# Performance work log

Hardware: AMD Instinct MI355X
Metric: run time of the kernel (lower is better)

Reference implementation:

```python
import jax, jax.numpy as jnp
import numpy as np
from jax import lax

B, S, I = 128, 256, 128          # batch, seq_len, input_size
CTX, OUT = 256, 128              # context_input_size, output_size
CPM, NM = 1024, 4                # center_size_per_module, num_modules
CENTER = NM * CPM
IN_SIZES = [I + CTX, CTX, CTX, CTX]          # only module 0 sees the input
HID = [CPM, CPM, CPM, CPM + OUT]             # last module also emits output


def setup_inputs() -> dict:
    key = jax.random.key(0)
    ks = jax.random.split(key, 4 + 5 * NM)
    d = {
        "inputs": jax.random.normal(ks[0], (B, 1, S, I), jnp.float32),
        "center_init": jax.random.normal(ks[1], (NM, B, CPM), jnp.float32),
        "mod_init": jax.random.normal(ks[2], (NM - 1, B, CPM), jnp.float32),
        "mod_init_last": jax.random.normal(ks[3], (B, CPM + OUT), jnp.float32),
    }
    for i in range(NM):
        k = ks[4 + 5 * i: 4 + 5 * (i + 1)]
        d[f"pm{i}"] = jax.random.normal(k[0], (CENTER, CTX), jnp.float32) * 0.02
        d[f"wih{i}"] = jax.random.normal(k[1], (3 * HID[i], IN_SIZES[i]), jnp.float32) * 0.05
        d[f"whh{i}"] = jax.random.normal(k[2], (3 * HID[i], HID[i]), jnp.float32) * 0.05
        d[f"bih{i}"] = jnp.zeros((3 * HID[i],), jnp.float32)
        d[f"bhh{i}"] = jnp.zeros((3 * HID[i],), jnp.float32)
    return d


def _gru(x, h, wih, whh, bih, bhh):
    # PyTorch GRUCell semantics
    gi = x @ wih.T + bih
    gh = h @ whh.T + bhh
    ir, iz, inn = jnp.split(gi, 3, axis=1)
    hr, hz, hn = jnp.split(gh, 3, axis=1)
    r = jax.nn.sigmoid(ir + hr)
    z = jax.nn.sigmoid(iz + hz)
    n = jnp.tanh(inn + r * hn)
    return (1.0 - z) * n + z * h


def _forward(inputs, center_init, mod_init, mod_init_last, pms, wihs, whhs, bihs, bhhs):
    xs = jnp.swapaxes(inputs[:, 0], 0, 1)  # [S, B, I]

    def step(carry, x_t):
        centers, mods, mod_last = carry  # [NM,B,CPM], [NM-1,B,CPM], [B,CPM+OUT]
        # torch.cat(prev_center_states, dim=1): module-major concat -> [B, NM*CPM]
        center_state = jnp.reshape(jnp.swapaxes(centers, 0, 1), (centers.shape[1], -1))
        new_centers, new_mods = [], []
        out = new_mod_last = None
        for i in range(NM):
            ctx = center_state @ pms[i]                       # [B, CTX]
            xin = jnp.concatenate([x_t, ctx], axis=1) if i == 0 else ctx
            h_prev = mod_last if i == NM - 1 else mods[i]
            h = _gru(xin, h_prev, wihs[i], whhs[i], bihs[i], bhhs[i])
            if i == NM - 1:
                out = h[:, :OUT]                              # split([output, center_feat])
                new_centers.append(h[:, OUT:])
                new_mod_last = h
            else:
                new_centers.append(h)
                new_mods.append(h)
        return (jnp.stack(new_centers), jnp.stack(new_mods), new_mod_last), out

    _, ys = lax.scan(step, (center_init, mod_init, mod_init_last), xs)
    return jnp.swapaxes(ys, 0, 1)  # [B, S, OUT]


def reference(inputs, center_init, mod_init, mod_init_last,
              pm0, pm1, pm2, pm3,
              wih0, wih1, wih2, wih3,
              whh0, whh1, whh2, whh3,
              bih0, bih1, bih2, bih3,
              bhh0, bhh1, bhh2, bhh3):
    return _forward(inputs, center_init, mod_init, mod_init_last,
                    (pm0, pm1, pm2, pm3),
                    (wih0, wih1, wih2, wih3),
                    (whh0, whh1, whh2, whh3),
                    (bih0, bih1, bih2, bih3),
                    (bhh0, bhh1, bhh2, bhh3))
```

## Files before the change

### kernel.cpp

```cpp
#include <hip/hip_runtime.h>
#include <hip/hip_bf16.h>

typedef _Float16 f16;
typedef f16  f16x8 __attribute__((ext_vector_type(8)));
typedef float f32x4 __attribute__((ext_vector_type(4)));

__device__ __forceinline__ f16x8 ld8h(const f16* p){ return *reinterpret_cast<const f16x8*>(p); }
__device__ __forceinline__ void fsplit(float x, f16* hi, f16* lo){
    f16 h=(f16)x; *hi=h; *lo=(f16)((x-(float)h)*4096.0f);
}
__device__ __forceinline__ size_t fragoff(int n, int k, int Kc){
    return ((size_t)(n>>4)*Kc + (k>>5))*512 + (size_t)((((k&31)>>3)*16 + (n&15))*8 + (k&7));
}

constexpr size_t NXE   = 128ull*256*128;
constexpr size_t NPM   = 1024ull*4096;
constexpr size_t NWIH0 = 3072ull*384;
constexpr size_t NWIH12= 3072ull*256;
constexpr size_t NWIH3 = 3456ull*256;
constexpr size_t NWHH  = 3072ull*1024;
constexpr size_t NWHH3 = 3456ull*1152;
constexpr size_t NCEN  = 128ull*4096;
constexpr size_t NCTX  = 128ull*1024;
constexpr size_t NHMX  = 128ull*1152;

constexpr size_t OFF_XH    = 0;
constexpr size_t OFF_XL    = OFF_XH + NXE*2;
constexpr size_t OFF_PMH   = OFF_XL + NXE*2;
constexpr size_t OFF_PML   = OFF_PMH + NPM*2;
constexpr size_t OFF_WIHH0 = OFF_PML + NPM*2;
constexpr size_t OFF_WIHH1 = OFF_WIHH0 + NWIH0*2;
constexpr size_t OFF_WIHH2 = OFF_WIHH1 + NWIH12*2;
constexpr size_t OFF_WIHH3 = OFF_WIHH2 + NWIH12*2;
constexpr size_t OFF_WIHL0 = OFF_WIHH3 + NWIH3*2;
constexpr size_t OFF_WIHL1 = OFF_WIHL0 + NWIH0*2;
constexpr size_t OFF_WIHL2 = OFF_WIHL1 + NWIH12*2;
constexpr size_t OFF_WIHL3 = OFF_WIHL2 + NWIH12*2;
constexpr size_t OFF_WHHH0 = OFF_WIHL3 + NWIH3*2;
constexpr size_t OFF_WHHH1 = OFF_WHHH0 + NWHH*2;
constexpr size_t OFF_WHHH2 = OFF_WHHH1 + NWHH*2;
constexpr size_t OFF_WHHH3 = OFF_WHHH2 + NWHH*2;
constexpr size_t OFF_WHHL0 = OFF_WHHH3 + NWHH3*2;
constexpr size_t OFF_WHHL1 = OFF_WHHL0 + NWHH*2;
constexpr size_t OFF_WHHL2 = OFF_WHHL1 + NWHH*2;
constexpr size_t OFF_WHHL3 = OFF_WHHL2 + NWHH*2;
constexpr size_t OFF_CENH  = OFF_WHHL3 + NWHH3*2;
constexpr size_t OFF_CENL  = OFF_CENH + 2*NCEN*2;
constexpr size_t OFF_CTXH  = OFF_CENL + 2*NCEN*2;
constexpr size_t OFF_CTXL  = OFF_CTXH + NCTX*2;
constexpr size_t OFF_HH    = OFF_CTXL + NCTX*2;
constexpr size_t OFF_HL    = OFF_HH + 8*NHMX*2;
constexpr size_t OFF_HF    = OFF_HL + 8*NHMX*2;
constexpr size_t WS_NEED   = OFF_HF + 8*NHMX*4;

__device__ __forceinline__ f16* hh_ptr(char* ws,int p,int i){ return (f16*)(ws+OFF_HH+((size_t)(p*4+i))*NHMX*2); }
__device__ __forceinline__ f16* hl_ptr(char* ws,int p,int i){ return (f16*)(ws+OFF_HL+((size_t)(p*4+i))*NHMX*2); }
__device__ __forceinline__ float* hf_ptr(char* ws,int p,int i){ return (float*)(ws+OFF_HF+((size_t)(p*4+i))*NHMX*4); }

__global__ void k_repack_w(const float* __restrict__ src, f16* __restrict__ hi,
                           f16* __restrict__ lo, int K){
    int n = blockIdx.x;
    const float* row = src + (size_t)n*K;
    int Kc = K >> 5;
    for (int k8 = threadIdx.x*8; k8 < K; k8 += 2048) {
        f16x8 hv, lv;
        #pragma unroll
        for (int e = 0; e < 8; ++e) { f16 a,b; fsplit(row[k8+e], &a, &b); hv[e]=a; lv[e]=b; }
        size_t d = fragoff(n, k8, Kc);
        *reinterpret_cast<f16x8*>(hi + d) = hv;
        *reinterpret_cast<f16x8*>(lo + d) = lv;
    }
}

__global__ void k_repack_pm(const float* __restrict__ p0, const float* __restrict__ p1,
                            const float* __restrict__ p2, const float* __restrict__ p3,
                            f16* __restrict__ hi, f16* __restrict__ lo){
    int k0 = blockIdx.x * 8;
    for (int c = threadIdx.x; c < 1024; c += 256) {
        int i = c >> 8, nl = c & 255;
        const float* p = (i==0?p0 : i==1?p1 : i==2?p2 : p3);
        f16x8 hv, lv;
        #pragma unroll
        for (int e = 0; e < 8; ++e) { f16 a,b; fsplit(p[(size_t)(k0+e)*256 + nl], &a, &b); hv[e]=a; lv[e]=b; }
        #pragma unroll
        for (int e = 0; e < 8; ++e) { size_t d = fragoff(c, k0+e, 128); hi[d]=hv[e]; lo[d]=lv[e]; }
    }
}

__global__ void k_repack_x(const float* __restrict__ src, f16* __restrict__ hi, f16* __restrict__ lo){
    size_t g = ((size_t)blockIdx.x*256 + threadIdx.x) * 8;
    if (g >= NXE) return;
    int m = (int)(g >> 15), t = (int)((g >> 7) & 255), d0 = (int)(g & 127);
    f16x8 hv, lv;
    #pragma unroll
    for (int e = 0; e < 8; ++e) { f16 a,b; fsplit(src[g+e], &a, &b); hv[e]=a; lv[e]=b; }
    size_t d = (size_t)t*16384 + fragoff(m, d0, 4);
    *reinterpret_cast<f16x8*>(hi + d) = hv;
    *reinterpret_cast<f16x8*>(lo + d) = lv;
}

__global__ void k_init_cen(const float* __restrict__ ci, char* ws){
    size_t g = ((size_t)blockIdx.x*256 + threadIdx.x) * 8;
    if (g >= 4ull*128*1024) return;
    int i = (int)(g >> 17), b = (int)((g >> 10) & 127), c = (int)(g & 1023);
    f16* hi = (f16*)(ws + OFF_CENH);
    f16* lo = (f16*)(ws + OFF_CENL);
    f16x8 hv, lv;
    #pragma unroll
    for (int e = 0; e < 8; ++e) { f16 a,bb; fsplit(ci[g+e], &a, &bb); hv[e]=a; lv[e]=bb; }
    size_t d = fragoff(b, i*1024 + c, 128);
    *reinterpret_cast<f16x8*>(hi + d) = hv;
    *reinterpret_cast<f16x8*>(lo + d) = lv;
}

__global__ void k_init_mod(const float* __restrict__ mi, char* ws){
    size_t g = ((size_t)blockIdx.x*256 + threadIdx.x) * 8;
    if (g >= 3ull*128*1024) return;
    int i = (int)(g >> 17), b = (int)((g >> 10) & 127), j = (int)(g & 1023);
    float* hf = hf_ptr(ws, 0, i);
    f16 *hh = hh_ptr(ws, 0, i), *hl = hl_ptr(ws, 0, i);
    f16x8 hv, lv;
    #pragma unroll
    for (int e = 0; e < 8; ++e) {
        float v = mi[g+e]; hf[(size_t)b*1024 + j + e] = v;
        f16 a,bb; fsplit(v, &a, &bb); hv[e]=a; lv[e]=bb;
    }
    size_t d = fragoff(b, j, 32);
    *reinterpret_cast<f16x8*>(hh + d) = hv;
    *reinterpret_cast<f16x8*>(hl + d) = lv;
}

__global__ void k_init_last(const float* __restrict__ ml, char* ws){
    int b = blockIdx.x;
    float* hf = hf_ptr(ws, 0, 3);
    f16 *hh = hh_ptr(ws, 0, 3), *hl = hl_ptr(ws, 0, 3);
    for (int j = threadIdx.x*8; j < 1152; j += 2048) {
        f16x8 hv, lv;
        #pragma unroll
        for (int e = 0; e < 8; ++e) {
            float v = ml[(size_t)b*1152 + j + e]; hf[(size_t)b*1152 + j + e] = v;
            f16 a,bb; fsplit(v, &a, &bb); hv[e]=a; lv[e]=bb;
        }
        size_t d = fragoff(b, j, 36);
        *reinterpret_cast<f16x8*>(hh + d) = hv;
        *reinterpret_cast<f16x8*>(hl + d) = lv;
    }
}

__global__ __launch_bounds__(512) void k_ctx(char* ws, int par){
    __shared__ float red[8][32][17];
    const f16* cenh = (const f16*)(ws + OFF_CENH) + (size_t)par*NCEN;
    const f16* cenl = (const f16*)(ws + OFF_CENL) + (size_t)par*NCEN;
    const f16* pmh  = (const f16*)(ws + OFF_PMH);
    const f16* pml  = (const f16*)(ws + OFF_PML);
    int tid = threadIdx.x, lane = tid & 63, wv = tid >> 6;
    int bm = blockIdx.x >> 6, bn = blockIdx.x & 63;
    size_t lb = (size_t)lane*8;
    size_t a0 = ((size_t)(bm*2)*128 + wv*16)*512 + lb;
    size_t a1 = a0 + 128*512;
    size_t bb = ((size_t)bn*128 + wv*16)*512 + lb;
    f32x4 h0={},h1={},c0={},c1={};
    #pragma unroll 4
    for (int kc = 0; kc < 16; ++kc) {
        f16x8 bh = ld8h(pmh + bb + kc*512), bl = ld8h(pml + bb + kc*512);
        f16x8 ah0 = ld8h(cenh + a0 + kc*512), al0 = ld8h(cenl + a0 + kc*512);
        f16x8 ah1 = ld8h(cenh + a1 + kc*512), al1 = ld8h(cenl + a1 + kc*512);
        h0 = __builtin_amdgcn_mfma_f32_16x16x32_f16(ah0, bh, h0, 0,0,0);
        c0 = __builtin_amdgcn_mfma_f32_16x16x32_f16(al0, bh, c0, 0,0,0);
        c0 = __builtin_amdgcn_mfma_f32_16x16x32_f16(ah0, bl, c0, 0,0,0);
        h1 = __builtin_amdgcn_mfma_f32_16x16x32_f16(ah1, bh, h1, 0,0,0);
        c1 = __builtin_amdgcn_mfma_f32_16x16x32_f16(al1, bh, c1, 0,0,0);
        c1 = __builtin_amdgcn_mfma_f32_16x16x32_f16(ah1, bl, c1, 0,0,0);
    }
    int rg = lane >> 4, fr = lane & 15;
    const float inv = 1.0f/4096.0f;
    #pragma unroll
    for (int rr = 0; rr < 4; ++rr) {
        red[wv][rg*4+rr][fr]      = h0[rr] + c0[rr]*inv;
        red[wv][16+rg*4+rr][fr]   = h1[rr] + c1[rr]*inv;
    }
    __syncthreads();
    int r = tid >> 4, c = tid & 15;
    float s = red[0][r][c]+red[1][r][c]+red[2][r][c]+red[3][r][c]
            + red[4][r][c]+red[5][r][c]+red[6][r][c]+red[7][r][c];
    int m = bm*32 + r, n = bn*16 + c;
    size_t d = fragoff(m, n, 32);
    f16* ctxh = (f16*)(ws + OFF_CTXH);
    f16* ctxl = (f16*)(ws + OFF_CTXL);
    fsplit(s, &ctxh[d], &ctxl[d]);
}

__global__ __launch_bounds__(256) void k_fused(char* ws,
    const float* __restrict__ bih0, const float* __restrict__ bih1,
    const float* __restrict__ bih2, const float* __restrict__ bih3,
    const float* __restrict__ bhh0, const float* __restrict__ bhh1,
    const float* __restrict__ bhh2, const float* __restrict__ bhh3,
    float* __restrict__ out, int t, int par)
{
    int tid = threadIdx.x, lane = tid & 63, wv = tid >> 6;
    int fr = lane & 15, rg = lane >> 4;
    int tile = blockIdx.x;
    int i, jt;
    if (tile < 64)       { i = 0; jt = tile; }
    else if (tile < 128) { i = 1; jt = tile - 64; }
    else if (tile < 192) { i = 2; jt = tile - 128; }
    else                 { i = 3; jt = tile - 192; }
    const int H  = (i == 3) ? 1152 : 1024;
    const int K1 = (i == 0) ? 384 : 256;
    const int Kc1 = K1 >> 5, KcH = H >> 5, Ht = H >> 4;

    const f16* WihH = (const f16*)(ws + (i==0?OFF_WIHH0 : i==1?OFF_WIHH1 : i==2?OFF_WIHH2 : OFF_WIHH3));
    const f16* WihL = (const f16*)(ws + (i==0?OFF_WIHL0 : i==1?OFF_WIHL1 : i==2?OFF_WIHL2 : OFF_WIHL3));
    const f16* WhhH = (const f16*)(ws + (i==0?OFF_WHHH0 : i==1?OFF_WHHH1 : i==2?OFF_WHHH2 : OFF_WHHH3));
    const f16* WhhL = (const f16*)(ws + (i==0?OFF_WHHL0 : i==1?OFF_WHHL1 : i==2?OFF_WHHL2 : OFF_WHHL3));

    size_t lb = (size_t)lane*8;
    size_t b1[3], b2[3];
    #pragma unroll
    for (int s = 0; s < 3; ++s) {
        b1[s] = ((size_t)(s*Ht + jt)*Kc1)*512 + lb;
        b2[s] = ((size_t)(s*Ht + jt)*KcH)*512 + lb;
    }
    int mt0 = wv*2;
    f32x4 aRh[2]={{},{}}, aRc[2]={{},{}}, aZh[2]={{},{}}, aZc[2]={{},{}};
    f32x4 aIh[2]={{},{}}, aIc[2]={{},{}}, aNh[2]={{},{}}, aNc[2]={{},{}};

    {
        const f16* XH_ = (const f16*)(ws + OFF_XH);
        const f16* XL_ = (const f16*)(ws + OFF_XL);
        const f16* CH_ = (const f16*)(ws + OFF_CTXH);
        const f16* CL_ = (const f16*)(ws + OFF_CTXL);
        size_t xb0 = ((size_t)(t*8 + mt0)*4)*512 + lb, xb1 = xb0 + 4*512;
        size_t cb0 = ((size_t)mt0*32)*512 + lb,        cb1 = cb0 + 32*512;
        #pragma unroll 2
        for (int kc = 0; kc < Kc1; ++kc) {
            f16x8 ah0, al0, ah1, al1;
            if (i == 0 && kc < 4) {
                ah0 = ld8h(XH_ + xb0 + kc*512); al0 = ld8h(XL_ + xb0 + kc*512);
                ah1 = ld8h(XH_ + xb1 + kc*512); al1 = ld8h(XL_ + xb1 + kc*512);
            } else {
                int ck = (i == 0) ? kc - 4 : i*8 + kc;
                ah0 = ld8h(CH_ + cb0 + ck*512); al0 = ld8h(CL_ + cb0 + ck*512);
                ah1 = ld8h(CH_ + cb1 + ck*512); al1 = ld8h(CL_ + cb1 + ck*512);
            }
            f16x8 bh, bl;
            bh = ld8h(WihH + b1[0] + kc*512); bl = ld8h(WihL + b1[0] + kc*512);
            aRh[0] = __builtin_amdgcn_mfma_f32_16x16x32_f16(ah0, bh, aRh[0],0,0,0);
            aRc[0] = __builtin_amdgcn_mfma_f32_16x16x32_f16(al0, bh, aRc[0],0,0,0);
            aRc[0] = __builtin_amdgcn_mfma_f32_16x16x32_f16(ah0, bl, aRc[0],0,0,0);
            aRh[1] = __builtin_amdgcn_mfma_f32_16x16x32_f16(ah1, bh, aRh[1],0,0,0);
            aRc[1] = __builtin_amdgcn_mfma_f32_16x16x32_f16(al1, bh, aRc[1],0,0,0);
            aRc[1] = __builtin_amdgcn_mfma_f32_16x16x32_f16(ah1, bl, aRc[1],0,0,0);
            bh = ld8h(WihH + b1[1] + kc*512); bl = ld8h(WihL + b1[1] + kc*512);
            aZh[0] = __builtin_amdgcn_mfma_f32_16x16x32_f16(ah0, bh, aZh[0],0,0,0);
            aZc[0] = __builtin_amdgcn_mfma_f32_16x16x32_f16(al0, bh, aZc[0],0,0,0);
            aZc[0] = __builtin_amdgcn_mfma_f32_16x16x32_f16(ah0, bl, aZc[0],0,0,0);
            aZh[1] = __builtin_amdgcn_mfma_f32_16x16x32_f16(ah1, bh, aZh[1],0,0,0);
            aZc[1] = __builtin_amdgcn_mfma_f32_16x16x32_f16(al1, bh, aZc[1],0,0,0);
            aZc[1] = __builtin_amdgcn_mfma_f32_16x16x32_f16(ah1, bl, aZc[1],0,0,0);
            bh = ld8h(WihH + b1[2] + kc*512); bl = ld8h(WihL + b1[2] + kc*512);
            aIh[0] = __builtin_amdgcn_mfma_f32_16x16x32_f16(ah0, bh, aIh[0],0,0,0);
            aIc[0] = __builtin_amdgcn_mfma_f32_16x16x32_f16(al0, bh, aIc[0],0,0,0);
            aIc[0] = __builtin_amdgcn_mfma_f32_16x16x32_f16(ah0, bl, aIc[0],0,0,0);
            aIh[1] = __builtin_amdgcn_mfma_f32_16x16x32_f16(ah1, bh, aIh[1],0,0,0);
            aIc[1] = __builtin_amdgcn_mfma_f32_16x16x32_f16(al1, bh, aIc[1],0,0,0);
            aIc[1] = __builtin_amdgcn_mfma_f32_16x16x32_f16(ah1, bl, aIc[1],0,0,0);
        }
    }
    {
        const f16* HHp = hh_ptr(ws, par, i);
        const f16* HLp = hl_ptr(ws, par, i);
        size_t hb0 = ((size_t)mt0*KcH)*512 + lb, hb1 = hb0 + (size_t)KcH*512;
        #pragma unroll 2
        for (int kc = 0; kc < KcH; ++kc) {
            f16x8 ah0 = ld8h(HHp + hb0 + kc*512), al0 = ld8h(HLp + hb0 + kc*512);
            f16x8 ah1 = ld8h(HHp + hb1 + kc*512), al1 = ld8h(HLp + hb1 + kc*512);
            f16x8 bh, bl;
            bh = ld8h(WhhH + b2[0] + kc*512); bl = ld8h(WhhL + b2[0] + kc*512);
            aRh[0] = __builtin_amdgcn_mfma_f32_16x16x32_f16(ah0, bh, aRh[0],0,0,0);
            aRc[0] = __builtin_amdgcn_mfma_f32_16x16x32_f16(al0, bh, aRc[0],0,0,0);
            aRc[0] = __builtin_amdgcn_mfma_f32_16x16x32_f16(ah0, bl, aRc[0],0,0,0);
            aRh[1] = __builtin_amdgcn_mfma_f32_16x16x32_f16(ah1, bh, aRh[1],0,0,0);
            aRc[1] = __builtin_amdgcn_mfma_f32_16x16x32_f16(al1, bh, aRc[1],0,0,0);
            aRc[1] = __builtin_amdgcn_mfma_f32_16x16x32_f16(ah1, bl, aRc[1],0,0,0);
            bh = ld8h(WhhH + b2[1] + kc*512); bl = ld8h(WhhL + b2[1] + kc*512);
            aZh[0] = __builtin_amdgcn_mfma_f32_16x16x32_f16(ah0, bh, aZh[0],0,0,0);
            aZc[0] = __builtin_amdgcn_mfma_f32_16x16x32_f16(al0, bh, aZc[0],0,0,0);
            aZc[0] = __builtin_amdgcn_mfma_f32_16x16x32_f16(ah0, bl, aZc[0],0,0,0);
            aZh[1] = __builtin_amdgcn_mfma_f32_16x16x32_f16(ah1, bh, aZh[1],0,0,0);
            aZc[1] = __builtin_amdgcn_mfma_f32_16x16x32_f16(al1, bh, aZc[1],0,0,0);
            aZc[1] = __builtin_amdgcn_mfma_f32_16x16x32_f16(ah1, bl, aZc[1],0,0,0);
            bh = ld8h(WhhH + b2[2] + kc*512); bl = ld8h(WhhL + b2[2] + kc*512);
            aNh[0] = __builtin_amdgcn_mfma_f32_16x16x32_f16(ah0, bh, aNh[0],0,0,0);
            aNc[0] = __builtin_amdgcn_mfma_f32_16x16x32_f16(al0, bh, aNc[0],0,0,0);
            aNc[0] = __builtin_amdgcn_mfma_f32_16x16x32_f16(ah0, bl, aNc[0],0,0,0);
            aNh[1] = __builtin_amdgcn_mfma_f32_16x16x32_f16(ah1, bh, aNh[1],0,0,0);
            aNc[1] = __builtin_amdgcn_mfma_f32_16x16x32_f16(al1, bh, aNc[1],0,0,0);
            aNc[1] = __builtin_amdgcn_mfma_f32_16x16x32_f16(ah1, bl, aNc[1],0,0,0);
        }
    }

    const float* bihp = (i==0?bih0 : i==1?bih1 : i==2?bih2 : bih3);
    const float* bhhp = (i==0?bhh0 : i==1?bhh1 : i==2?bhh2 : bhh3);
    int j = jt*16 + fr;
    float bir = bihp[j], biz = bihp[H+j], bin = bihp[2*H+j];
    float bhr = bhhp[j], bhz = bhhp[H+j], bhn = bhhp[2*H+j];
    const float* hfP = hf_ptr(ws, par, i);
    float* hfN = hf_ptr(ws, par^1, i);
    f16 *hhN = hh_ptr(ws, par^1, i), *hlN = hl_ptr(ws, par^1, i);
    f16* cenhN = (f16*)(ws + OFF_CENH) + (size_t)(par^1)*NCEN;
    f16* cenlN = (f16*)(ws + OFF_CENL) + (size_t)(par^1)*NCEN;
    const float inv = 1.0f/4096.0f;
    #pragma unroll
    for (int mf = 0; mf < 2; ++mf) {
        #pragma unroll
        for (int rr = 0; rr < 4; ++rr) {
            float r_ = aRh[mf][rr] + aRc[mf][rr]*inv + bir + bhr;
            float z_ = aZh[mf][rr] + aZc[mf][rr]*inv + biz + bhz;
            float in_ = aIh[mf][rr] + aIc[mf][rr]*inv + bin;
            float hn_ = aNh[mf][rr] + aNc[mf][rr]*inv + bhn;
            float rgt = 1.f/(1.f + expf(-r_));
            float zgt = 1.f/(1.f + expf(-z_));
            float ngt = tanhf(in_ + rgt*hn_);
            int m = wv*32 + mf*16 + rg*4 + rr;
            float hp = hfP[(size_t)m*H + j];
            float hnew = (1.f - zgt)*ngt + zgt*hp;
            hfN[(size_t)m*H + j] = hnew;
            size_t hd = fragoff(m, j, KcH);
            fsplit(hnew, &hhN[hd], &hlN[hd]);
            if (i < 3) {
                size_t cd = fragoff(m, i*1024 + j, 128);
                fsplit(hnew, &cenhN[cd], &cenlN[cd]);
            } else if (j >= 128) {
                size_t cd = fragoff(m, 3072 + j - 128, 128);
                fsplit(hnew, &cenhN[cd], &cenlN[cd]);
            } else {
                out[((size_t)m*256 + t)*128 + j] = hnew;
            }
        }
    }
}

extern "C" void kernel_launch(void* const* d_in, const int* in_sizes, int n_in,
                              void* d_out, int out_size, void* d_ws, size_t ws_size,
                              hipStream_t stream)
{
    char* ws = (char*)d_ws;
    const float* inp   = (const float*)d_in[0];
    const float* cini  = (const float*)d_in[1];
    const float* mini  = (const float*)d_in[2];
    const float* mlast = (const float*)d_in[3];
    const float *pm[4], *wih[4], *whh[4], *bih[4], *bhh[4];
    for (int i = 0; i < 4; ++i) {
        pm[i]  = (const float*)d_in[4 + 5*i];
        wih[i] = (const float*)d_in[5 + 5*i];
        whh[i] = (const float*)d_in[6 + 5*i];
        bih[i] = (const float*)d_in[7 + 5*i];
        bhh[i] = (const float*)d_in[8 + 5*i];
    }
    float* out = (float*)d_out;

    k_repack_x<<<2048, 256, 0, stream>>>(inp, (f16*)(ws+OFF_XH), (f16*)(ws+OFF_XL));
    k_repack_pm<<<512, 256, 0, stream>>>(pm[0], pm[1], pm[2], pm[3],
                                         (f16*)(ws+OFF_PMH), (f16*)(ws+OFF_PML));
    k_repack_w<<<3072, 256, 0, stream>>>(wih[0], (f16*)(ws+OFF_WIHH0), (f16*)(ws+OFF_WIHL0), 384);
    k_repack_w<<<3072, 256, 0, stream>>>(wih[1], (f16*)(ws+OFF_WIHH1), (f16*)(ws+OFF_WIHL1), 256);
    k_repack_w<<<3072, 256, 0, stream>>>(wih[2], (f16*)(ws+OFF_WIHH2), (f16*)(ws+OFF_WIHL2), 256);
    k_repack_w<<<3456, 256, 0, stream>>>(wih[3], (f16*)(ws+OFF_WIHH3), (f16*)(ws+OFF_WIHL3), 256);
    k_repack_w<<<3072, 256, 0, stream>>>(whh[0], (f16*)(ws+OFF_WHHH0), (f16*)(ws+OFF_WHHL0), 1024);
    k_repack_w<<<3072, 256, 0, stream>>>(whh[1], (f16*)(ws+OFF_WHHH1), (f16*)(ws+OFF_WHHL1), 1024);
    k_repack_w<<<3072, 256, 0, stream>>>(whh[2], (f16*)(ws+OFF_WHHH2), (f16*)(ws+OFF_WHHL2), 1024);
    k_repack_w<<<3456, 256, 0, stream>>>(whh[3], (f16*)(ws+OFF_WHHH3), (f16*)(ws+OFF_WHHL3), 1152);
    k_init_cen<<<256, 256, 0, stream>>>(cini, ws);
    k_init_mod<<<192, 256, 0, stream>>>(mini, ws);
    k_init_last<<<128, 256, 0, stream>>>(mlast, ws);

    for (int t = 0; t < 256; ++t) {
        int par = t & 1;
        k_ctx<<<256, 512, 0, stream>>>(ws, par);
        k_fused<<<264, 256, 0, stream>>>(ws,
            bih[0], bih[1], bih[2], bih[3],
            bhh[0], bhh[1], bhh[2], bhh[3],
            out, t, par);
    }
    (void)in_sizes; (void)n_in; (void)out_size; (void)ws_size; (void)WS_NEED;
}
```

Before: 14.59 ms.

## Stage GRU weight tiles into LDS with double-buffered async global_load_lds

The fused GRU step kernel now copies weight fragments (hi/lo, three gates) into a double-buffered shared-memory tile using async global-to-LDS loads, overlapping the next stage's loads with the current stage's MFMAs. Each weight fragment is loaded once per block instead of once by each of the four waves. The two K loops (input and hidden) are merged into one staged loop with a barrier per stage. Launch bounds now request two blocks per CU. The added __syncthreads per stage may cost more than it saves given the small per-stage work. The pm repack kernel is also reordered slightly.

Result: slower. 24.33 ms (+66.7%).

```diff
diff --git a/kernel.cpp b/kernel.cpp
--- a/kernel.cpp
+++ b/kernel.cpp
@@ -9,8 +9,14 @@
 __device__ __forceinline__ void fsplit(float x, f16* hi, f16* lo){
     f16 h=(f16)x; *hi=h; *lo=(f16)((x-(float)h)*4096.0f);
 }
+#define MFMA16(a,b,c) __builtin_amdgcn_mfma_f32_16x16x32_f16((a),(b),(c),0,0,0)
 __device__ __forceinline__ size_t fragoff(int n, int k, int Kc){
     return ((size_t)(n>>4)*Kc + (k>>5))*512 + (size_t)((((k&31)>>3)*16 + (n&15))*8 + (k&7));
+}
+__device__ __forceinline__ void gl_lds16(const f16* g, f16* l){
+    __builtin_amdgcn_global_load_lds(
+        (const __attribute__((address_space(1))) void*)g,
+        (__attribute__((address_space(3))) void*)l, 16, 0, 0);
 }
 
 constexpr size_t NXE   = 128ull*256*128;
@@ -79,11 +85,11 @@
     for (int c = threadIdx.x; c < 1024; c += 256) {
         int i = c >> 8, nl = c & 255;
         const float* p = (i==0?p0 : i==1?p1 : i==2?p2 : p3);
-        f16x8 hv, lv;
-        #pragma unroll
-        for (int e = 0; e < 8; ++e) { f16 a,b; fsplit(p[(size_t)(k0+e)*256 + nl], &a, &b); hv[e]=a; lv[e]=b; }
-        #pragma unroll
-        for (int e = 0; e < 8; ++e) { size_t d = fragoff(c, k0+e, 128); hi[d]=hv[e]; lo[d]=lv[e]; }
+        #pragma unroll
+        for (int e = 0; e < 8; ++e) {
+            f16 a,b; fsplit(p[(size_t)(k0+e)*256 + nl], &a, &b);
+            size_t d = fragoff(c, k0+e, 128); hi[d]=a; lo[d]=b;
+        }
     }
 }
 
@@ -165,12 +171,8 @@
         f16x8 bh = ld8h(pmh + bb + kc*512), bl = ld8h(pml + bb + kc*512);
         f16x8 ah0 = ld8h(cenh + a0 + kc*512), al0 = ld8h(cenl + a0 + kc*512);
         f16x8 ah1 = ld8h(cenh + a1 + kc*512), al1 = ld8h(cenl + a1 + kc*512);
-        h0 = __builtin_amdgcn_mfma_f32_16x16x32_f16(ah0, bh, h0, 0,0,0);
-        c0 = __builtin_amdgcn_mfma_f32_16x16x32_f16(al0, bh, c0, 0,0,0);
-        c0 = __builtin_amdgcn_mfma_f32_16x16x32_f16(ah0, bl, c0, 0,0,0);
-        h1 = __builtin_amdgcn_mfma_f32_16x16x32_f16(ah1, bh, h1, 0,0,0);
-        c1 = __builtin_amdgcn_mfma_f32_16x16x32_f16(al1, bh, c1, 0,0,0);
-        c1 = __builtin_amdgcn_mfma_f32_16x16x32_f16(ah1, bl, c1, 0,0,0);
+        h0 = MFMA16(ah0,bh,h0); c0 = MFMA16(al0,bh,c0); c0 = MFMA16(ah0,bl,c0);
+        h1 = MFMA16(ah1,bh,h1); c1 = MFMA16(al1,bh,c1); c1 = MFMA16(ah1,bl,c1);
     }
     int rg = lane >> 4, fr = lane & 15;
     const float inv = 1.0f/4096.0f;
@@ -190,16 +192,17 @@
     fsplit(s, &ctxh[d], &ctxl[d]);
 }
 
-__global__ __launch_bounds__(256) void k_fused(char* ws,
+__global__ __launch_bounds__(256, 2) void k_fused(char* ws,
     const float* __restrict__ bih0, const float* __restrict__ bih1,
     const float* __restrict__ bih2, const float* __restrict__ bih3,
     const float* __restrict__ bhh0, const float* __restrict__ bhh1,
     const float* __restrict__ bhh2, const float* __restrict__ bhh3,
     float* __restrict__ out, int t, int par)
 {
-    int tid = threadIdx.x, lane = tid & 63, wv = tid >> 6;
-    int fr = lane & 15, rg = lane >> 4;
-    int tile = blockIdx.x;
+    __shared__ f16 Bs[2][3][2][1024];
+    const int tid = threadIdx.x, lane = tid & 63, wv = tid >> 6;
+    const int fr = lane & 15, rg = lane >> 4;
+    const int tile = blockIdx.x;
     int i, jt;
     if (tile < 64)       { i = 0; jt = tile; }
     else if (tile < 128) { i = 1; jt = tile - 64; }
@@ -208,103 +211,100 @@
     const int H  = (i == 3) ? 1152 : 1024;
     const int K1 = (i == 0) ? 384 : 256;
     const int Kc1 = K1 >> 5, KcH = H >> 5, Ht = H >> 4;
+    const int P1 = Kc1 >> 1, P = P1 + (KcH >> 1);
 
     const f16* WihH = (const f16*)(ws + (i==0?OFF_WIHH0 : i==1?OFF_WIHH1 : i==2?OFF_WIHH2 : OFF_WIHH3));
     const f16* WihL = (const f16*)(ws + (i==0?OFF_WIHL0 : i==1?OFF_WIHL1 : i==2?OFF_WIHL2 : OFF_WIHL3));
     const f16* WhhH = (const f16*)(ws + (i==0?OFF_WHHH0 : i==1?OFF_WHHH1 : i==2?OFF_WHHH2 : OFF_WHHH3));
     const f16* WhhL = (const f16*)(ws + (i==0?OFF_WHHL0 : i==1?OFF_WHHL1 : i==2?OFF_WHHL2 : OFF_WHHL3));
-
-    size_t lb = (size_t)lane*8;
     size_t b1[3], b2[3];
     #pragma unroll
     for (int s = 0; s < 3; ++s) {
-        b1[s] = ((size_t)(s*Ht + jt)*Kc1)*512 + lb;
-        b2[s] = ((size_t)(s*Ht + jt)*KcH)*512 + lb;
-    }
-    int mt0 = wv*2;
-    f32x4 aRh[2]={{},{}}, aRc[2]={{},{}}, aZh[2]={{},{}}, aZc[2]={{},{}};
-    f32x4 aIh[2]={{},{}}, aIc[2]={{},{}}, aNh[2]={{},{}}, aNc[2]={{},{}};
-
-    {
-        const f16* XH_ = (const f16*)(ws + OFF_XH);
-        const f16* XL_ = (const f16*)(ws + OFF_XL);
-        const f16* CH_ = (const f16*)(ws + OFF_CTXH);
-        const f16* CL_ = (const f16*)(ws + OFF_CTXL);
-        size_t xb0 = ((size_t)(t*8 + mt0)*4)*512 + lb, xb1 = xb0 + 4*512;
-        size_t cb0 = ((size_t)mt0*32)*512 + lb,        cb1 = cb0 + 32*512;
-        #pragma unroll 2
-        for (int kc = 0; kc < Kc1; ++kc) {
+        b1[s] = ((size_t)(s*Ht + jt)*Kc1)*512;
+        b2[s] = ((size_t)(s*Ht + jt)*KcH)*512;
+    }
+    const size_t lb = (size_t)lane*8;
+    const int mt0 = wv*2;
+    const f16* XH_ = (const f16*)(ws + OFF_XH);
+    const f16* XL_ = (const f16*)(ws + OFF_XL);
+    const f16* CH_ = (const f16*)(ws + OFF_CTXH);
+    const f16* CL_ = (const f16*)(ws + OFF_CTXL);
+    const f16* HHp = hh_ptr(ws, par, i);
+    const f16* HLp = hl_ptr(ws, par, i);
+    const size_t xb0 = ((size_t)(t*8 + mt0)*4)*512 + lb, xb1 = xb0 + 2048;
+    const size_t cb0 = ((size_t)mt0*32)*512 + lb,        cb1 = cb0 + 16384;
+    const size_t hb0 = ((size_t)mt0*KcH)*512 + lb,       hb1 = hb0 + (size_t)KcH*512;
+
+    f32x4 rh[2]={{},{}}, rc[2]={{},{}}, zh[2]={{},{}}, zc[2]={{},{}};
+    f32x4 inh[2]={{},{}}, inc[2]={{},{}}, nhh[2]={{},{}}, nhc[2]={{},{}};
+
+    auto stage = [&](int p){
+        const int buf = p & 1;
+        const bool ih = p < P1;
+        const int lp = ih ? p : p - P1;
+        #pragma unroll
+        for (int q = 0; q < 3; ++q) {
+            const int c = wv*3 + q;
+            const int s = c >> 2, a = (c >> 1) & 1, hlf = c & 1;
+            const f16* base = ih ? (a ? WihL : WihH) : (a ? WhhL : WhhH);
+            const size_t off = (ih ? b1[s] : b2[s]) + (size_t)lp*1024 + (size_t)hlf*512 + lb;
+            gl_lds16(base + off, &Bs[buf][s][a][hlf*512]);
+        }
+    };
+
+    auto compute = [&](int p){
+        const int buf = p & 1;
+        const bool ih = p < P1;
+        const int lp = ih ? p : p - P1;
+        #pragma unroll
+        for (int kl = 0; kl < 2; ++kl) {
+            const int kc = lp*2 + kl;
             f16x8 ah0, al0, ah1, al1;
-            if (i == 0 && kc < 4) {
-                ah0 = ld8h(XH_ + xb0 + kc*512); al0 = ld8h(XL_ + xb0 + kc*512);
-                ah1 = ld8h(XH_ + xb1 + kc*512); al1 = ld8h(XL_ + xb1 + kc*512);
+            if (ih) {
+                if (i == 0 && kc < 4) {
+                    ah0 = ld8h(XH_ + xb0 + kc*512); al0 = ld8h(XL_ + xb0 + kc*512);
+                    ah1 = ld8h(XH_ + xb1 + kc*512); al1 = ld8h(XL_ + xb1 + kc*512);
+                } else {
+                    const int ck = (i == 0) ? kc - 4 : i*8 + kc;
+                    ah0 = ld8h(CH_ + cb0 + ck*512); al0 = ld8h(CL_ + cb0 + ck*512);
+                    ah1 = ld8h(CH_ + cb1 + ck*512); al1 = ld8h(CL_ + cb1 + ck*512);
+                }
             } else {
-                int ck = (i == 0) ? kc - 4 : i*8 + kc;
-                ah0 = ld8h(CH_ + cb0 + ck*512); al0 = ld8h(CL_ + cb0 + ck*512);
-                ah1 = ld8h(CH_ + cb1 + ck*512); al1 = ld8h(CL_ + cb1 + ck*512);
+                ah0 = ld8h(HHp + hb0 + kc*512); al0 = ld8h(HLp + hb0 + kc*512);
+                ah1 = ld8h(HHp + hb1 + kc*512); al1 = ld8h(HLp + hb1 + kc*512);
             }
+            const f16* bsl = &Bs[buf][0][0][kl*512 + lane*8];
             f16x8 bh, bl;
-            bh = ld8h(WihH + b1[0] + kc*512); bl = ld8h(WihL + b1[0] + kc*512);
-            aRh[0] = __builtin_amdgcn_mfma_f32_16x16x32_f16(ah0, bh, aRh[0],0,0,0);
-            aRc[0] = __builtin_amdgcn_mfma_f32_16x16x32_f16(al0, bh, aRc[0],0,0,0);
-            aRc[0] = __builtin_amdgcn_mfma_f32_16x16x32_f16(ah0, bl, aRc[0],0,0,0);
-            aRh[1] = __builtin_amdgcn_mfma_f32_16x16x32_f16(ah1, bh, aRh[1],0,0,0);
-            aRc[1] = __builtin_amdgcn_mfma_f32_16x16x32_f16(al1, bh, aRc[1],0,0,0);
-            aRc[1] = __builtin_amdgcn_mfma_f32_16x16x32_f16(ah1, bl, aRc[1],0,0,0);
-            bh = ld8h(WihH + b1[1] + kc*512); bl = ld8h(WihL + b1[1] + kc*512);
-            aZh[0] = __builtin_amdgcn_mfma_f32_16x16x32_f16(ah0, bh, aZh[0],0,0,0);
-            aZc[0] = __builtin_amdgcn_mfma_f32_16x16x32_f16(al0, bh, aZc[0],0,0,0);
-            aZc[0] = __builtin_amdgcn_mfma_f32_16x16x32_f16(ah0, bl, aZc[0],0,0,0);
-            aZh[1] = __builtin_amdgcn_mfma_f32_16x16x32_f16(ah1, bh, aZh[1],0,0,0);
-            aZc[1] = __builtin_amdgcn_mfma_f32_16x16x32_f16(al1, bh, aZc[1],0,0,0);
-            aZc[1] = __builtin_amdgcn_mfma_f32_16x16x32_f16(ah1, bl, aZc[1],0,0,0);
-            bh = ld8h(WihH + b1[2] + kc*512); bl = ld8h(WihL + b1[2] + kc*512);
-            aIh[0] = __builtin_amdgcn_mfma_f32_16x16x32_f16(ah0, bh, aIh[0],0,0,0);
-            aIc[0] = __builtin_amdgcn_mfma_f32_16x16x32_f16(al0, bh, aIc[0],0,0,0);
-            aIc[0] = __builtin_amdgcn_mfma_f32_16x16x32_f16(ah0, bl, aIc[0],0,0,0);
-            aIh[1] = __builtin_amdgcn_mfma_f32_16x16x32_f16(ah1, bh, aIh[1],0,0,0);
-            aIc[1] = __builtin_amdgcn_mfma_f32_16x16x32_f16(al1, bh, aIc[1],0,0,0);
-            aIc[1] = __builtin_amdgcn_mfma_f32_16x16x32_f16(ah1, bl, aIc[1],0,0,0);
-        }
-    }
-    {
-        const f16* HHp = hh_ptr(ws, par, i);
-        const f16* HLp = hl_ptr(ws, par, i);
-        size_t hb0 = ((size_t)mt0*KcH)*512 + lb, hb1 = hb0 + (size_t)KcH*512;
-        #pragma unroll 2
-        for (int kc = 0; kc < KcH; ++kc) {
-            f16x8 ah0 = ld8h(HHp + hb0 + kc*512), al0 = ld8h(HLp + hb0 + kc*512);
-            f16x8 ah1 = ld8h(HHp + hb1 + kc*512), al1 = ld8h(HLp + hb1 + kc*512);
-            f16x8 bh, bl;
-            bh = ld8h(WhhH + b2[0] + kc*512); bl = ld8h(WhhL + b2[0] + kc*512);
-            aRh[0] = __builtin_amdgcn_mfma_f32_16x16x32_f16(ah0, bh, aRh[0],0,0,0);
-            aRc[0] = __builtin_amdgcn_mfma_f32_16x16x32_f16(al0, bh, aRc[0],0,0,0);
-            aRc[0] = __builtin_amdgcn_mfma_f32_16x16x32_f16(ah0, bl, aRc[0],0,0,0);
-            aRh[1] = __builtin_amdgcn_mfma_f32_16x16x32_f16(ah1, bh, aRh[1],0,0,0);
-            aRc[1] = __builtin_amdgcn_mfma_f32_16x16x32_f16(al1, bh, aRc[1],0,0,0);
-            aRc[1] = __builtin_amdgcn_mfma_f32_16x16x32_f16(ah1, bl, aRc[1],0,0,0);
-            bh = ld8h(WhhH + b2[1] + kc*512); bl = ld8h(WhhL + b2[1] + kc*512);
-            aZh[0] = __builtin_amdgcn_mfma_f32_16x16x32_f16(ah0, bh, aZh[0],0,0,0);
-            aZc[0] = __builtin_amdgcn_mfma_f32_16x16x32_f16(al0, bh, aZc[0],0,0,0);
-            aZc[0] = __builtin_amdgcn_mfma_f32_16x16x32_f16(ah0, bl, aZc[0],0,0,0);
-            aZh[1] = __builtin_amdgcn_mfma_f32_16x16x32_f16(ah1, bh, aZh[1],0,0,0);
-            aZc[1] = __builtin_amdgcn_mfma_f32_16x16x32_f16(al1, bh, aZc[1],0,0,0);
-            aZc[1] = __builtin_amdgcn_mfma_f32_16x16x32_f16(ah1, bl, aZc[1],0,0,0);
-            bh = ld8h(WhhH + b2[2] + kc*512); bl = ld8h(WhhL + b2[2] + kc*512);
-            aNh[0] = __builtin_amdgcn_mfma_f32_16x16x32_f16(ah0, bh, aNh[0],0,0,0);
-            aNc[0] = __builtin_amdgcn_mfma_f32_16x16x32_f16(al0, bh, aNc[0],0,0,0);
-            aNc[0] = __builtin_amdgcn_mfma_f32_16x16x32_f16(ah0, bl, aNc[0],0,0,0);
-            aNh[1] = __builtin_amdgcn_mfma_f32_16x16x32_f16(ah1, bh, aNh[1],0,0,0);
-            aNc[1] = __builtin_amdgcn_mfma_f32_16x16x32_f16(al1, bh, aNc[1],0,0,0);
-            aNc[1] = __builtin_amdgcn_mfma_f32_16x16x32_f16(ah1, bl, aNc[1],0,0,0);
-        }
+            bh = *(const f16x8*)(bsl);          bl = *(const f16x8*)(bsl + 1024);
+            rh[0]=MFMA16(ah0,bh,rh[0]); rc[0]=MFMA16(al0,bh,rc[0]); rc[0]=MFMA16(ah0,bl,rc[0]);
+            rh[1]=MFMA16(ah1,bh,rh[1]); rc[1]=MFMA16(al1,bh,rc[1]); rc[1]=MFMA16(ah1,bl,rc[1]);
+            bh = *(const f16x8*)(bsl + 2048);   bl = *(const f16x8*)(bsl + 3072);
+            zh[0]=MFMA16(ah0,bh,zh[0]); zc[0]=MFMA16(al0,bh,zc[0]); zc[0]=MFMA16(ah0,bl,zc[0]);
+            zh[1]=MFMA16(ah1,bh,zh[1]); zc[1]=MFMA16(al1,bh,zc[1]); zc[1]=MFMA16(ah1,bl,zc[1]);
+            bh = *(const f16x8*)(bsl + 4096);   bl = *(const f16x8*)(bsl + 5120);
+            if (ih) {
+                inh[0]=MFMA16(ah0,bh,inh[0]); inc[0]=MFMA16(al0,bh,inc[0]); inc[0]=MFMA16(ah0,bl,inc[0]);
+                inh[1]=MFMA16(ah1,bh,inh[1]); inc[1]=MFMA16(al1,bh,inc[1]); inc[1]=MFMA16(ah1,bl,inc[1]);
+            } else {
+                nhh[0]=MFMA16(ah0,bh,nhh[0]); nhc[0]=MFMA16(al0,bh,nhc[0]); nhc[0]=MFMA16(ah0,bl,nhc[0]);
+                nhh[1]=MFMA16(ah1,bh,nhh[1]); nhc[1]=MFMA16(al1,bh,nhc[1]); nhc[1]=MFMA16(ah1,bl,nhc[1]);
+            }
+        }
+    };
+
+    stage(0);
+    __syncthreads();
+    for (int p = 0; p < P; ++p) {
+        if (p + 1 < P) stage(p + 1);
+        compute(p);
+        __syncthreads();
     }
 
     const float* bihp = (i==0?bih0 : i==1?bih1 : i==2?bih2 : bih3);
     const float* bhhp = (i==0?bhh0 : i==1?bhh1 : i==2?bhh2 : bhh3);
-    int j = jt*16 + fr;
-    float bir = bihp[j], biz = bihp[H+j], bin = bihp[2*H+j];
-    float bhr = bhhp[j], bhz = bhhp[H+j], bhn = bhhp[2*H+j];
+    const int j = jt*16 + fr;
+    const float bir = bihp[j], biz = bihp[H+j], bin = bihp[2*H+j];
+    const float bhr = bhhp[j], bhz = bhhp[H+j], bhn = bhhp[2*H+j];
     const float* hfP = hf_ptr(ws, par, i);
     float* hfN = hf_ptr(ws, par^1, i);
     f16 *hhN = hh_ptr(ws, par^1, i), *hlN = hl_ptr(ws, par^1, i);
@@ -315,10 +315,10 @@
     for (int mf = 0; mf < 2; ++mf) {
         #pragma unroll
         for (int rr = 0; rr < 4; ++rr) {
-            float r_ = aRh[mf][rr] + aRc[mf][rr]*inv + bir + bhr;
-            float z_ = aZh[mf][rr] + aZc[mf][rr]*inv + biz + bhz;
-            float in_ = aIh[mf][rr] + aIc[mf][rr]*inv + bin;
-            float hn_ = aNh[mf][rr] + aNc[mf][rr]*inv + bhn;
+            float r_  = rh[mf][rr]  + rc[mf][rr]*inv  + bir + bhr;
+            float z_  = zh[mf][rr]  + zc[mf][rr]*inv  + biz + bhz;
+            float in_ = inh[mf][rr] + inc[mf][rr]*inv + bin;
+            float hn_ = nhh[mf][rr] + nhc[mf][rr]*inv + bhn;
             float rgt = 1.f/(1.f + expf(-r_));
             float zgt = 1.f/(1.f + expf(-z_));
             float ngt = tanhf(in_ + rgt*hn_);
```
